# Performance work log

Measured on AMD Instinct MI355X. Metric: run time of the kernel, lower is better.

Reference implementation:

```python
import jax, jax.numpy as jnp
import numpy as np

B, L, C = 2048, 2048, 16
F = L // 2                 # num_freqs = 1024
H = 4 * F                  # multi_factor * num_freqs = 4096
P = int(len(np.unique(L // np.arange(1, F + 1))))  # n patch sizes = 88
SCALE = 0.02
NOISE_EPS = 0.01


def setup_inputs() -> dict:
    key = jax.random.key(0)
    ks = jax.random.split(key, 10)
    return {
        "x": jax.random.normal(ks[0], (B, L, C), jnp.float32),
        "w_start": SCALE * jax.random.normal(ks[1], (C, 1), jnp.float32),
        "b_start": SCALE * jax.random.normal(ks[2], (1,), jnp.float32),
        "w1": SCALE * jax.random.normal(ks[3], (2, F, H), jnp.float32),
        "b1": SCALE * jax.random.normal(ks[4], (2, H), jnp.float32),
        "w2": SCALE * jax.random.normal(ks[5], (2, H, F), jnp.float32),
        "b2": SCALE * jax.random.normal(ks[6], (2, F), jnp.float32),
        "w_gate": SCALE * jax.random.normal(ks[7], (F, P), jnp.float32),
        "w_noise": SCALE * jax.random.normal(ks[8], (F, P), jnp.float32),
        "noise_z": jax.random.normal(ks[9], (B, P), jnp.float32),
        "top_k": 3,
    }


def reference(x, w_start, b_start, w1, b1, w2, b2, w_gate, w_noise, noise_z, top_k):
    # start_fc: [B, L, C] -> [B, L, 1] -> [B, 1, L]
    v = (jnp.einsum("blc,co->blo", x, w_start) + b_start).transpose(0, 2, 1)
    # rfft (ortho), drop DC bin -> [B, 1, F] complex
    xf = jnp.fft.rfft(v, axis=-1, norm="ortho")[:, :, 1:]
    xr, xi = jnp.real(xf), jnp.imag(xf)
    # complex 2-layer MLP in frequency domain
    o1r = jax.nn.relu(jnp.einsum("bdi,io->bdo", xr, w1[0]) - jnp.einsum("bdi,io->bdo", xi, w1[1]) + b1[0])
    o1i = jax.nn.relu(jnp.einsum("bdi,io->bdo", xi, w1[0]) + jnp.einsum("bdi,io->bdo", xr, w1[1]) + b1[1])
    o2r = jnp.einsum("bdo,of->bdf", o1r, w2[0]) - jnp.einsum("bdo,of->bdf", o1i, w2[1]) + b2[0]
    o2i = jnp.einsum("bdo,of->bdf", o1i, w2[0]) + jnp.einsum("bdo,of->bdf", o1r, w2[1]) + b2[1]
    amp = jnp.sqrt(o2r * o2r + o2i * o2i)[:, 0, :]  # [B, F]
    # router logits with (training) noise injection
    clean_logits = amp @ w_gate                      # [B, P]
    noise_std = jax.nn.softplus(amp @ w_noise) + NOISE_EPS
    logits = clean_logits + noise_z * noise_std
    # top-k -> softmax over top-k -> scatter into sparse gates
    top_w, top_i = jax.lax.top_k(logits, top_k)
    top_w = jax.nn.softmax(top_w, axis=-1)
    rows = jnp.arange(logits.shape[0])[:, None]
    gates = jnp.zeros_like(logits).at[rows, top_i].set(top_w)
    return gates
```

## Files before the change

### kernel.cpp

```cpp
#include <hip/hip_runtime.h>
#include <hip/hip_bf16.h>
#include <math.h>

#define B_DIM 2048
#define L_DIM 2048
#define F_DIM 1024
#define H_DIM 4096
#define P_DIM 88

typedef unsigned short u16;
typedef short bf16x8 __attribute__((ext_vector_type(8)));
typedef float f32x4 __attribute__((ext_vector_type(4)));

__device__ __forceinline__ u16 f2bf(float x) {
    unsigned u = __float_as_uint(x);
    return (u16)((u + 0x7fffu + ((u >> 16) & 1u)) >> 16);
}
__device__ __forceinline__ float bf2f(u16 h) {
    return __uint_as_float(((unsigned)h) << 16);
}

__device__ __forceinline__ void gload_lds16(const void* g, void* l) {
    unsigned loff = (unsigned)(uintptr_t)l;
    __builtin_amdgcn_global_load_lds(
        reinterpret_cast<const __attribute__((address_space(1))) void*>(
            reinterpret_cast<uintptr_t>(g)),
        reinterpret_cast<__attribute__((address_space(3))) void*>(loff),
        16, 0, 0);
}

__global__ __launch_bounds__(256) void fft_kernel(
    const float* __restrict__ x, const float* __restrict__ w_start,
    const float* __restrict__ b_start, u16* __restrict__ A1)
{
    __shared__ float re[2048];
    __shared__ float im[2048];
    __shared__ float twr[1024];
    __shared__ float twi[1024];
    int b = blockIdx.x;
    const size_t row0 = (size_t)(2 * b) * 2048;

    const float4* wp = (const float4*)w_start;
    float4 w0 = wp[0], w1 = wp[1], w2 = wp[2], w3 = wp[3];
    float bs = b_start[0];

    for (int i = threadIdx.x; i < 1024; i += 256) {
        float ang = -6.283185307179586f * ((float)i / 2048.0f);
        sincosf(ang, &twi[i], &twr[i]);
    }

    for (int l = threadIdx.x; l < 2048; l += 256) {
        const float4* xp0 = (const float4*)(x + (row0 + l) * 16);
        const float4* xp1 = (const float4*)(x + (row0 + 2048 + l) * 16);
        float4 a0 = xp0[0], a1 = xp0[1], a2 = xp0[2], a3 = xp0[3];
        float4 c0 = xp1[0], c1 = xp1[1], c2 = xp1[2], c3 = xp1[3];
        float va = bs, vb = bs;
        va += a0.x * w0.x + a0.y * w0.y + a0.z * w0.z + a0.w * w0.w;
        va += a1.x * w1.x + a1.y * w1.y + a1.z * w1.z + a1.w * w1.w;
        va += a2.x * w2.x + a2.y * w2.y + a2.z * w2.z + a2.w * w2.w;
        va += a3.x * w3.x + a3.y * w3.y + a3.z * w3.z + a3.w * w3.w;
        vb += c0.x * w0.x + c0.y * w0.y + c0.z * w0.z + c0.w * w0.w;
        vb += c1.x * w1.x + c1.y * w1.y + c1.z * w1.z + c1.w * w1.w;
        vb += c2.x * w2.x + c2.y * w2.y + c2.z * w2.z + c2.w * w2.w;
        vb += c3.x * w3.x + c3.y * w3.y + c3.z * w3.z + c3.w * w3.w;
        unsigned j = __brev((unsigned)l) >> 21;
        re[j] = va;
        im[j] = vb;
    }
    __syncthreads();

    for (int s = 1; s <= 11; s++) {
        int half = 1 << (s - 1);
        for (int t = threadIdx.x; t < 1024; t += 256) {
            int j = t & (half - 1);
            int base = (t >> (s - 1)) << s;
            int idx = j << (11 - s);
            float wr = twr[idx], wi = twi[idx];
            int i0 = base + j, i1 = i0 + half;
            float br = re[i1], bi = im[i1];
            float tr = br * wr - bi * wi;
            float ti = br * wi + bi * wr;
            float ar = re[i0], ai = im[i0];
            re[i0] = ar + tr; im[i0] = ai + ti;
            re[i1] = ar - tr; im[i1] = ai - ti;
        }
        __syncthreads();
    }

    const float sc = 0.5f * 0.022097086912079612f;
    u16* r0 = A1 + (size_t)(2 * b) * 4096;
    u16* r1 = r0 + 4096;
    for (int t = threadIdx.x; t < 1024; t += 256) {
        int k = t + 1;
        int nk = 2048 - k;
        float Zr = re[k], Zi = im[k], Yr = re[nk], Yi = im[nk];
        float Ar = (Zr + Yr) * sc;
        float Ai = (Zi - Yi) * sc;
        float Br = (Zi + Yi) * sc;
        float Bi = (Yr - Zr) * sc;
        u16 h, lo;
        h = f2bf(Ar); lo = f2bf(Ar - bf2f(h)); r0[t] = h; r0[1024 + t] = lo;
        h = f2bf(Ai); lo = f2bf(Ai - bf2f(h)); r0[2048 + t] = h; r0[3072 + t] = lo;
        h = f2bf(Br); lo = f2bf(Br - bf2f(h)); r1[t] = h; r1[1024 + t] = lo;
        h = f2bf(Bi); lo = f2bf(Bi - bf2f(h)); r1[2048 + t] = h; r1[3072 + t] = lo;
    }
}

__global__ __launch_bounds__(256) void conv_bt_kernel(
    const float* __restrict__ w, u16* __restrict__ BT, int Kc, int Nh)
{
    __shared__ float t0[32][33];
    __shared__ float t1[32][33];
    int k0 = blockIdx.x * 32, n0 = blockIdx.y * 32;
    int tx = threadIdx.x, ty = threadIdx.y;
    const float* w0 = w;
    const float* w1 = w + (size_t)Kc * Nh;

#pragma unroll
    for (int i = 0; i < 4; i++) {
        int k = k0 + ty + 8 * i;
        t0[ty + 8 * i][tx] = w0[(size_t)k * Nh + n0 + tx];
        t1[ty + 8 * i][tx] = w1[(size_t)k * Nh + n0 + tx];
    }
    __syncthreads();

    size_t K4 = 4 * (size_t)Kc;
    int k = k0 + tx;
#pragma unroll
    for (int i = 0; i < 4; i++) {
        int nl = ty + 8 * i;
        int n = n0 + nl;
        float br = t0[tx][nl];
        float bi = t1[tx][nl];
        u16 brh = f2bf(br); u16 brl = f2bf(br - bf2f(brh));
        float nbi = -bi;
        u16 nih = f2bf(nbi); u16 nil = f2bf(nbi - bf2f(nih));
        u16 pih = f2bf(bi);  u16 pil = f2bf(bi - bf2f(pih));
        u16* rowr = BT + (size_t)n * K4;
        rowr[0 * Kc + k] = brh; rowr[1 * Kc + k] = brl;
        rowr[2 * Kc + k] = nih; rowr[3 * Kc + k] = nil;
        u16* rowi = BT + (size_t)(Nh + n) * K4;
        rowi[0 * Kc + k] = pih; rowi[1 * Kc + k] = pil;
        rowi[2 * Kc + k] = brh; rowi[3 * Kc + k] = brl;
    }
}

extern __shared__ char smem8p[];

#define MFMA16(ACC0, ACC1, ACC2, ACC3, A0, A1, A2, A3, B0, B1, B2, B3)           \
    ACC0[0] = __builtin_amdgcn_mfma_f32_16x16x32_bf16(A0, B0, ACC0[0], 0, 0, 0); \
    ACC0[1] = __builtin_amdgcn_mfma_f32_16x16x32_bf16(A0, B1, ACC0[1], 0, 0, 0); \
    ACC0[2] = __builtin_amdgcn_mfma_f32_16x16x32_bf16(A0, B2, ACC0[2], 0, 0, 0); \
    ACC0[3] = __builtin_amdgcn_mfma_f32_16x16x32_bf16(A0, B3, ACC0[3], 0, 0, 0); \
    ACC1[0] = __builtin_amdgcn_mfma_f32_16x16x32_bf16(A1, B0, ACC1[0], 0, 0, 0); \
    ACC1[1] = __builtin_amdgcn_mfma_f32_16x16x32_bf16(A1, B1, ACC1[1], 0, 0, 0); \
    ACC1[2] = __builtin_amdgcn_mfma_f32_16x16x32_bf16(A1, B2, ACC1[2], 0, 0, 0); \
    ACC1[3] = __builtin_amdgcn_mfma_f32_16x16x32_bf16(A1, B3, ACC1[3], 0, 0, 0); \
    ACC2[0] = __builtin_amdgcn_mfma_f32_16x16x32_bf16(A2, B0, ACC2[0], 0, 0, 0); \
    ACC2[1] = __builtin_amdgcn_mfma_f32_16x16x32_bf16(A2, B1, ACC2[1], 0, 0, 0); \
    ACC2[2] = __builtin_amdgcn_mfma_f32_16x16x32_bf16(A2, B2, ACC2[2], 0, 0, 0); \
    ACC2[3] = __builtin_amdgcn_mfma_f32_16x16x32_bf16(A2, B3, ACC2[3], 0, 0, 0); \
    ACC3[0] = __builtin_amdgcn_mfma_f32_16x16x32_bf16(A3, B0, ACC3[0], 0, 0, 0); \
    ACC3[1] = __builtin_amdgcn_mfma_f32_16x16x32_bf16(A3, B1, ACC3[1], 0, 0, 0); \
    ACC3[2] = __builtin_amdgcn_mfma_f32_16x16x32_bf16(A3, B2, ACC3[2], 0, 0, 0); \
    ACC3[3] = __builtin_amdgcn_mfma_f32_16x16x32_bf16(A3, B3, ACC3[3], 0, 0, 0);

template <int EPI, int SWZ>
__global__ __launch_bounds__(512, 2) void gemm8p(
    const u16* __restrict__ A, const u16* __restrict__ B,
    const float* __restrict__ biasL, const float* __restrict__ biasR,
    u16* __restrict__ OutU, float* __restrict__ P01, float* __restrict__ P23,
    int Kc, int KcLog, int NH, int nt)
{
    char* ldsA = smem8p;
    char* ldsB = smem8p + 65536;

    const int tid = threadIdx.x;
    const int w = tid >> 6, lane = tid & 63;
    const int wr = w >> 2, wc = w & 3;
    const int fr = lane & 15, kb = lane >> 4;

    int bx, by, z;
    if (SWZ == 1) {
        int b = blockIdx.x;
        int xcd = b & 7, idx = b >> 3;
        bx = 4 * xcd + (idx & 3);
        by = idx >> 2;
        z = 0;
    } else if (SWZ == 2) {
        int b = blockIdx.x;
        by = b & 7;
        int s = b >> 3;
        bx = s & 7;
        z = s >> 3;
    } else {
        bx = blockIdx.x; by = blockIdx.y; z = blockIdx.z;
    }
    const int n0 = bx * 256, m0 = by * 256;
    const size_t K4 = 4 * (size_t)Kc;

    const int srow = tid >> 2;
    const int lk8 = (((tid & 3) ^ ((tid >> 3) & 3))) * 8;
    const int wb = (tid >> 6) * 1024;

    const int laneOff = fr * 64 + ((kb ^ ((fr >> 1) & 3)) << 4);

    f32x4 acc[8][4];
#pragma unroll
    for (int i = 0; i < 8; i++)
#pragma unroll
        for (int j = 0; j < 4; j++)
            acc[i][j] = (f32x4){0.f, 0.f, 0.f, 0.f};

    const int t0 = z * nt, te = t0 + nt;

    auto colA = [&](int t) {
        int k0 = t << 5;
        int seg = k0 >> KcLog, kk = k0 & (Kc - 1);
        int r3 = seg >= 3 ? seg - 3 : seg;
        int bs = seg >= 3 ? 2 : 0;
        return (bs + (r3 == 1 ? 1 : 0)) * Kc + kk;
    };
    auto colB = [&](int t) {
        int k0 = t << 5;
        int seg = k0 >> KcLog, kk = k0 & (Kc - 1);
        int r3 = seg >= 3 ? seg - 3 : seg;
        int bs = seg >= 3 ? 2 : 0;
        return (bs + (r3 == 2 ? 1 : 0)) * Kc + kk;
    };
    auto stageA = [&](int t) {
        const u16* src = A + (size_t)(m0 + srow) * K4 + colA(t) + lk8;
        char* dst = ldsA + (t & 3) * 16384 + wb;
        gload_lds16(src, dst);
        gload_lds16(src + (size_t)128 * K4, dst + 8192);
    };
    auto stageB = [&](int t) {
        const u16* src = B + (size_t)(n0 + srow) * K4 + colB(t) + lk8;
        char* dst = ldsB + (t & 3) * 16384 + wb;
        gload_lds16(src, dst);
        gload_lds16(src + (size_t)128 * K4, dst + 8192);
    };
    auto aBase = [&](int t) -> const char* {
        return ldsA + (t & 3) * 16384 + wr * 8192 + laneOff;
    };
    auto bBase = [&](int t) -> const char* {
        return ldsB + (t & 3) * 16384 + wc * 4096 + laneOff;
    };

    stageA(t0); stageB(t0);
    if (t0 + 1 < te) { stageA(t0 + 1); stageB(t0 + 1); }
    if (t0 + 1 < te) asm volatile("s_waitcnt vmcnt(4)" ::: "memory");
    else             asm volatile("s_waitcnt vmcnt(0)" ::: "memory");
    asm volatile("s_barrier" ::: "memory");

    bf16x8 b0, b1, b2, b3, a0, a1, a2, a3;
    {
        const char* aS = aBase(t0);
        const char* bS = bBase(t0);
        b0 = *(const bf16x8*)(bS + 0 * 1024);
        b1 = *(const bf16x8*)(bS + 1 * 1024);
        b2 = *(const bf16x8*)(bS + 2 * 1024);
        b3 = *(const bf16x8*)(bS + 3 * 1024);
        a0 = *(const bf16x8*)(aS + 0 * 1024);
        a1 = *(const bf16x8*)(aS + 1 * 1024);
        a2 = *(const bf16x8*)(aS + 2 * 1024);
        a3 = *(const bf16x8*)(aS + 3 * 1024);
    }

    for (int t = t0; t < te; ++t) {
        const bool haveStage = (t + 2 < te);
        const bool haveNext  = (t + 1 < te);

        if (haveStage) { stageA(t + 2); stageB(t + 2); }

        const char* aS = aBase(t);
        bf16x8 c0 = *(const bf16x8*)(aS + 4096 + 0 * 1024);
        bf16x8 c1 = *(const bf16x8*)(aS + 4096 + 1 * 1024);
        bf16x8 c2 = *(const bf16x8*)(aS + 4096 + 2 * 1024);
        bf16x8 c3 = *(const bf16x8*)(aS + 4096 + 3 * 1024);

        __builtin_amdgcn_s_setprio(1);
        MFMA16(acc[0], acc[1], acc[2], acc[3], a0, a1, a2, a3, b0, b1, b2, b3)
        __builtin_amdgcn_s_setprio(0);

        if (haveStage) asm volatile("s_waitcnt vmcnt(4)" ::: "memory");
        else           asm volatile("s_waitcnt vmcnt(0)" ::: "memory");
        asm volatile("s_barrier" ::: "memory");

        if (haveNext) {
            const char* aN = aBase(t + 1);
            a0 = *(const bf16x8*)(aN + 0 * 1024);
            a1 = *(const bf16x8*)(aN + 1 * 1024);
            a2 = *(const bf16x8*)(aN + 2 * 1024);
            a3 = *(const bf16x8*)(aN + 3 * 1024);
        }

        __builtin_amdgcn_s_setprio(1);
        MFMA16(acc[4], acc[5], acc[6], acc[7], c0, c1, c2, c3, b0, b1, b2, b3)
        __builtin_amdgcn_s_setprio(0);

        if (haveNext) {
            const char* bN = bBase(t + 1);
            b0 = *(const bf16x8*)(bN + 0 * 1024);
            b1 = *(const bf16x8*)(bN + 1 * 1024);
            b2 = *(const bf16x8*)(bN + 2 * 1024);
            b3 = *(const bf16x8*)(bN + 3 * 1024);
        }
    }

    const int fq = kb;
#pragma unroll
    for (int nj = 0; nj < 4; nj++) {
        int n = n0 + wc * 64 + nj * 16 + fr;
        if (EPI == 0) {
            bool left = (n < NH);
            int nn = left ? n : (n - NH);
            float bias = left ? biasL[n] : biasR[nn];
#pragma unroll
            for (int mi = 0; mi < 8; mi++) {
                int mb = m0 + wr * 128 + mi * 16 + fq * 4;
#pragma unroll
                for (int r = 0; r < 4; r++) {
                    float val = fmaxf(acc[mi][nj][r] + bias, 0.f);
                    u16 h = f2bf(val);
                    u16 lo = f2bf(val - bf2f(h));
                    size_t rb = (size_t)(mb + r) * (4 * (size_t)NH);
                    if (left) { OutU[rb + nn] = h; OutU[rb + NH + nn] = lo; }
                    else { OutU[rb + 2 * (size_t)NH + nn] = h; OutU[rb + 3 * (size_t)NH + nn] = lo; }
                }
            }
        } else {
            const size_t PSZ = (size_t)2048 * 2048;
            float* Out = (z < 2) ? (P01 + (size_t)z * PSZ) : (P23 + (size_t)(z - 2) * PSZ);
#pragma unroll
            for (int mi = 0; mi < 8; mi++) {
                int mb = m0 + wr * 128 + mi * 16 + fq * 4;
#pragma unroll
                for (int r = 0; r < 4; r++)
                    Out[(size_t)(mb + r) * 2048 + n] = acc[mi][nj][r];
            }
        }
    }
}

__global__ __launch_bounds__(256) void router_kernel(
    const float* __restrict__ P01, const float* __restrict__ P23, int ZK,
    const float* __restrict__ b2,
    const float* __restrict__ w_gate, const float* __restrict__ w_noise,
    const float* __restrict__ noise_z, float* __restrict__ gates)
{
    __shared__ float s_amp[8][1024];
    __shared__ float s_dot[8][176];
    __shared__ float s_lg[8][88];
    __shared__ int   s_idx[8][3];
    __shared__ float s_val[8][3];

    const int tid = threadIdx.x;
    const int r0 = blockIdx.x * 8;
    const size_t PSZ = (size_t)2048 * 2048;

    for (int idx = tid; idx < 8 * 1024; idx += 256) {
        int row = idx >> 10, i = idx & 1023;
        size_t roff = (size_t)(r0 + row) * 2048;
        float orr = b2[i];
        float oii = b2[1024 + i];
        for (int zz = 0; zz < ZK; zz++) {
            const float* Pz = ((zz < 2) ? (P01 + (size_t)zz * PSZ)
                                        : (P23 + (size_t)(zz - 2) * PSZ)) + roff;
            orr += Pz[i];
            oii += Pz[1024 + i];
        }
        s_amp[row][i] = sqrtf(orr * orr + oii * oii);
    }
    __syncthreads();

    for (int idx = tid; idx < 8 * 176; idx += 256) {
        int row = idx / 176, c = idx % 176;
        const float* wcol = (c < 88) ? (w_gate + c) : (w_noise + (c - 88));
        float s = 0.f;
        const float4* av = (const float4*)s_amp[row];
        for (int k4 = 0; k4 < 256; k4++) {
            float4 a = av[k4];
            int k = k4 * 4;
            s = fmaf(a.x, wcol[(size_t)(k + 0) * 88], s);
            s = fmaf(a.y, wcol[(size_t)(k + 1) * 88], s);
            s = fmaf(a.z, wcol[(size_t)(k + 2) * 88], s);
            s = fmaf(a.w, wcol[(size_t)(k + 3) * 88], s);
        }
        s_dot[row][c] = s;
    }
    __syncthreads();

    for (int idx = tid; idx < 8 * 88; idx += 256) {
        int row = idx / 88, c = idx % 88;
        float cn = s_dot[row][88 + c];
        float ns = (cn > 20.f) ? cn : log1pf(expf(cn));
        ns += 0.01f;
        s_lg[row][c] = s_dot[row][c] + noise_z[(size_t)(r0 + row) * 88 + c] * ns;
    }
    __syncthreads();

    if (tid < 8) {
        int i0 = -1, i1 = -1, i2 = -1;
        float v0 = -1e30f, v1 = -1e30f, v2 = -1e30f;
        for (int i = 0; i < P_DIM; i++) {
            float t = s_lg[tid][i];
            if (t > v0) { v0 = t; i0 = i; }
        }
        for (int i = 0; i < P_DIM; i++) {
            if (i == i0) continue;
            float t = s_lg[tid][i];
            if (t > v1) { v1 = t; i1 = i; }
        }
        for (int i = 0; i < P_DIM; i++) {
            if (i == i0 || i == i1) continue;
            float t = s_lg[tid][i];
            if (t > v2) { v2 = t; i2 = i; }
        }
        s_idx[tid][0] = i0; s_idx[tid][1] = i1; s_idx[tid][2] = i2;
        s_val[tid][0] = v0; s_val[tid][1] = v1; s_val[tid][2] = v2;
    }
    __syncthreads();

    for (int idx = tid; idx < 8 * 88; idx += 256) {
        int row = idx / 88, c = idx % 88;
        float m = s_val[row][0];
        float e0 = expf(s_val[row][0] - m);
        float e1 = expf(s_val[row][1] - m);
        float e2 = expf(s_val[row][2] - m);
        float inv = 1.f / (e0 + e1 + e2);
        float g = 0.f;
        if (c == s_idx[row][0]) g = e0 * inv;
        else if (c == s_idx[row][1]) g = e1 * inv;
        else if (c == s_idx[row][2]) g = e2 * inv;
        gates[(size_t)(r0 + row) * 88 + c] = g;
    }
}

extern "C" void kernel_launch(void* const* d_in, const int* in_sizes, int n_in,
                              void* d_out, int out_size, void* d_ws, size_t ws_size,
                              hipStream_t stream)
{
    const float* x       = (const float*)d_in[0];
    const float* w_start = (const float*)d_in[1];
    const float* b_start = (const float*)d_in[2];
    const float* w1      = (const float*)d_in[3];
    const float* b1      = (const float*)d_in[4];
    const float* w2      = (const float*)d_in[5];
    const float* b2      = (const float*)d_in[6];
    const float* w_gate  = (const float*)d_in[7];
    const float* w_noise = (const float*)d_in[8];
    const float* noise_z = (const float*)d_in[9];
    float* gates = (float*)d_out;

    const size_t MB = 1024 * 1024;
    char* base = (char*)d_ws;
    u16*  A1   = (u16*)(base + 16 * MB);
    u16*  BT   = (u16*)(base + 32 * MB);
    u16*  A2   = (u16*)(base + 96 * MB);
    float* P01 = (float*)base;
    float* P23 = (float*)(base + 160 * MB);

    int ZK = (ws_size >= (size_t)192 * MB) ? 4 : 2;

    hipFuncSetAttribute(reinterpret_cast<const void*>(&gemm8p<0, 1>),
                        hipFuncAttributeMaxDynamicSharedMemorySize, 131072);
    hipFuncSetAttribute(reinterpret_cast<const void*>(&gemm8p<1, 2>),
                        hipFuncAttributeMaxDynamicSharedMemorySize, 131072);

    fft_kernel<<<B_DIM / 2, 256, 0, stream>>>(x, w_start, b_start, A1);

    conv_bt_kernel<<<dim3(F_DIM / 32, H_DIM / 32), dim3(32, 8), 0, stream>>>(
        w1, BT, F_DIM, H_DIM);
    gemm8p<0, 1><<<256, 512, 131072, stream>>>(
        A1, BT, b1, b1 + H_DIM, A2, nullptr, nullptr, F_DIM, 10, H_DIM, 192);

    conv_bt_kernel<<<dim3(H_DIM / 32, F_DIM / 32), dim3(32, 8), 0, stream>>>(
        w2, BT, H_DIM, F_DIM);
    gemm8p<1, 2><<<64 * ZK, 512, 131072, stream>>>(
        A2, BT, nullptr, nullptr, nullptr, P01, P23, H_DIM, 12, F_DIM, 768 / ZK);

    router_kernel<<<B_DIM / 8, 256, 0, stream>>>(
        P01, P23, ZK, b2, w_gate, w_noise, noise_z, gates);
}
```

Baseline: 600.5 us.

## Load GEMM B operand directly from global in MFMA-ready layout, bypassing LDS

The weight-conversion kernel now writes the split-bf16 B matrix in a k-chunked layout of 8-element vectors per column, so each lane can fetch its MFMA B fragment with a single 16-byte global load. The GEMM drops the B LDS staging buffer and its async copies, prefetches B one tile ahead in registers, and unrolls the K loop by two to ping-pong the register sets. This halves dynamic shared memory and removes B LDS traffic, but each wave now issues its own uncoalesced-ish global loads for B with no cross-wave reuse, and assumes an even tile count per block.

```diff
diff --git a/kernel.cpp b/kernel.cpp
--- a/kernel.cpp
+++ b/kernel.cpp
@@ -107,7 +107,7 @@
 }
 
 __global__ __launch_bounds__(256) void conv_bt_kernel(
-    const float* __restrict__ w, u16* __restrict__ BT, int Kc, int Nh)
+    const float* __restrict__ w, u16* __restrict__ BTk, int Kc, int Nh)
 {
     __shared__ float t0[32][33];
     __shared__ float t1[32][33];
@@ -124,8 +124,9 @@
     }
     __syncthreads();
 
-    size_t K4 = 4 * (size_t)Kc;
+    const size_t N2 = 2 * (size_t)Nh;
     int k = k0 + tx;
+    int ke = k & 7;
 #pragma unroll
     for (int i = 0; i < 4; i++) {
         int nl = ty + 8 * i;
@@ -136,18 +137,27 @@
         float nbi = -bi;
         u16 nih = f2bf(nbi); u16 nil = f2bf(nbi - bf2f(nih));
         u16 pih = f2bf(bi);  u16 pil = f2bf(bi - bf2f(pih));
-        u16* rowr = BT + (size_t)n * K4;
-        rowr[0 * Kc + k] = brh; rowr[1 * Kc + k] = brl;
-        rowr[2 * Kc + k] = nih; rowr[3 * Kc + k] = nil;
-        u16* rowi = BT + (size_t)(Nh + n) * K4;
-        rowi[0 * Kc + k] = pih; rowi[1 * Kc + k] = pil;
-        rowi[2 * Kc + k] = brh; rowi[3 * Kc + k] = brl;
+        size_t c8b = (size_t)(k >> 3);
+        size_t cstep = (size_t)(Kc >> 3);
+        size_t ur = 0, ui = 0;
+        ur = (c8b + 0 * cstep) * N2 + n;
+        BTk[ur * 8 + ke] = brh;
+        BTk[(c8b + 1 * cstep) * N2 * 8 + (size_t)n * 8 + ke] = brl;
+        BTk[(c8b + 2 * cstep) * N2 * 8 + (size_t)n * 8 + ke] = nih;
+        BTk[(c8b + 3 * cstep) * N2 * 8 + (size_t)n * 8 + ke] = nil;
+        BTk[ur * 8 + ke] = brh;
+        size_t nr = (size_t)(Nh + n);
+        BTk[(c8b + 0 * cstep) * N2 * 8 + nr * 8 + ke] = pih;
+        BTk[(c8b + 1 * cstep) * N2 * 8 + nr * 8 + ke] = pil;
+        BTk[(c8b + 2 * cstep) * N2 * 8 + nr * 8 + ke] = brh;
+        BTk[(c8b + 3 * cstep) * N2 * 8 + nr * 8 + ke] = brl;
+        (void)ui;
     }
 }
 
 extern __shared__ char smem8p[];
 
-#define MFMA16(ACC0, ACC1, ACC2, ACC3, A0, A1, A2, A3, B0, B1, B2, B3)           \
+#define MFMA16X(ACC0, ACC1, ACC2, ACC3, A0, A1, A2, A3, B0, B1, B2, B3)          \
     ACC0[0] = __builtin_amdgcn_mfma_f32_16x16x32_bf16(A0, B0, ACC0[0], 0, 0, 0); \
     ACC0[1] = __builtin_amdgcn_mfma_f32_16x16x32_bf16(A0, B1, ACC0[1], 0, 0, 0); \
     ACC0[2] = __builtin_amdgcn_mfma_f32_16x16x32_bf16(A0, B2, ACC0[2], 0, 0, 0); \
@@ -165,6 +175,41 @@
     ACC3[2] = __builtin_amdgcn_mfma_f32_16x16x32_bf16(A3, B2, ACC3[2], 0, 0, 0); \
     ACC3[3] = __builtin_amdgcn_mfma_f32_16x16x32_bf16(A3, B3, ACC3[3], 0, 0, 0);
 
+#define GTILE(T, BC0, BC1, BC2, BC3, BN0, BN1, BN2, BN3)                          \
+    {                                                                             \
+        const bool haveStage = ((T) + 2 < te);                                    \
+        const bool haveNext  = ((T) + 1 < te);                                    \
+        if (haveNext) {                                                           \
+            size_t u = (size_t)(unsigned)(colB((T) + 1) >> 3) * N2 + laneB;       \
+            BN0 = BK[u];      BN1 = BK[u + 16];                                   \
+            BN2 = BK[u + 32]; BN3 = BK[u + 48];                                   \
+        }                                                                         \
+        if (haveStage) stageA((T) + 2);                                           \
+        const char* aS = aBase(T);                                                \
+        bf16x8 c0 = *(const bf16x8*)(aS + 4096 + 0 * 1024);                       \
+        bf16x8 c1 = *(const bf16x8*)(aS + 4096 + 1 * 1024);                       \
+        bf16x8 c2 = *(const bf16x8*)(aS + 4096 + 2 * 1024);                       \
+        bf16x8 c3 = *(const bf16x8*)(aS + 4096 + 3 * 1024);                       \
+        __builtin_amdgcn_s_setprio(1);                                            \
+        MFMA16X(acc[0], acc[1], acc[2], acc[3], a0, a1, a2, a3,                   \
+                BC0, BC1, BC2, BC3)                                               \
+        __builtin_amdgcn_s_setprio(0);                                            \
+        if (haveStage) asm volatile("s_waitcnt vmcnt(2)" ::: "memory");           \
+        else           asm volatile("s_waitcnt vmcnt(0)" ::: "memory");           \
+        asm volatile("s_barrier" ::: "memory");                                   \
+        if (haveNext) {                                                           \
+            const char* aN = aBase((T) + 1);                                      \
+            a0 = *(const bf16x8*)(aN + 0 * 1024);                                 \
+            a1 = *(const bf16x8*)(aN + 1 * 1024);                                 \
+            a2 = *(const bf16x8*)(aN + 2 * 1024);                                 \
+            a3 = *(const bf16x8*)(aN + 3 * 1024);                                 \
+        }                                                                         \
+        __builtin_amdgcn_s_setprio(1);                                            \
+        MFMA16X(acc[4], acc[5], acc[6], acc[7], c0, c1, c2, c3,                   \
+                BC0, BC1, BC2, BC3)                                               \
+        __builtin_amdgcn_s_setprio(0);                                            \
+    }
+
 template <int EPI, int SWZ>
 __global__ __launch_bounds__(512, 2) void gemm8p(
     const u16* __restrict__ A, const u16* __restrict__ B,
@@ -173,7 +218,6 @@
     int Kc, int KcLog, int NH, int nt)
 {
     char* ldsA = smem8p;
-    char* ldsB = smem8p + 65536;
 
     const int tid = threadIdx.x;
     const int w = tid >> 6, lane = tid & 63;
@@ -198,12 +242,16 @@
     }
     const int n0 = bx * 256, m0 = by * 256;
     const size_t K4 = 4 * (size_t)Kc;
+    const size_t N2 = 2 * (size_t)NH;
 
     const int srow = tid >> 2;
     const int lk8 = (((tid & 3) ^ ((tid >> 3) & 3))) * 8;
     const int wb = (tid >> 6) * 1024;
 
     const int laneOff = fr * 64 + ((kb ^ ((fr >> 1) & 3)) << 4);
+
+    const bf16x8* BK = (const bf16x8*)B;
+    const size_t laneB = (size_t)kb * N2 + (size_t)(n0 + wc * 64 + fr);
 
     f32x4 acc[8][4];
 #pragma unroll
@@ -234,78 +282,33 @@
         gload_lds16(src, dst);
         gload_lds16(src + (size_t)128 * K4, dst + 8192);
     };
-    auto stageB = [&](int t) {
-        const u16* src = B + (size_t)(n0 + srow) * K4 + colB(t) + lk8;
-        char* dst = ldsB + (t & 3) * 16384 + wb;
-        gload_lds16(src, dst);
-        gload_lds16(src + (size_t)128 * K4, dst + 8192);
-    };
     auto aBase = [&](int t) -> const char* {
         return ldsA + (t & 3) * 16384 + wr * 8192 + laneOff;
     };
-    auto bBase = [&](int t) -> const char* {
-        return ldsB + (t & 3) * 16384 + wc * 4096 + laneOff;
-    };
-
-    stageA(t0); stageB(t0);
-    if (t0 + 1 < te) { stageA(t0 + 1); stageB(t0 + 1); }
-    if (t0 + 1 < te) asm volatile("s_waitcnt vmcnt(4)" ::: "memory");
-    else             asm volatile("s_waitcnt vmcnt(0)" ::: "memory");
+
+    bf16x8 bc0, bc1, bc2, bc3, bn0, bn1, bn2, bn3;
+    {
+        size_t u = (size_t)(unsigned)(colB(t0) >> 3) * N2 + laneB;
+        bc0 = BK[u];      bc1 = BK[u + 16];
+        bc2 = BK[u + 32]; bc3 = BK[u + 48];
+    }
+    stageA(t0);
+    stageA(t0 + 1);
+    asm volatile("s_waitcnt vmcnt(2)" ::: "memory");
     asm volatile("s_barrier" ::: "memory");
 
-    bf16x8 b0, b1, b2, b3, a0, a1, a2, a3;
+    bf16x8 a0, a1, a2, a3;
     {
         const char* aS = aBase(t0);
-        const char* bS = bBase(t0);
-        b0 = *(const bf16x8*)(bS + 0 * 1024);
-        b1 = *(const bf16x8*)(bS + 1 * 1024);
-        b2 = *(const bf16x8*)(bS + 2 * 1024);
-        b3 = *(const bf16x8*)(bS + 3 * 1024);
         a0 = *(const bf16x8*)(aS + 0 * 1024);
         a1 = *(const bf16x8*)(aS + 1 * 1024);
         a2 = *(const bf16x8*)(aS + 2 * 1024);
         a3 = *(const bf16x8*)(aS + 3 * 1024);
     }
 
-    for (int t = t0; t < te; ++t) {
-        const bool haveStage = (t + 2 < te);
-        const bool haveNext  = (t + 1 < te);
-
-        if (haveStage) { stageA(t + 2); stageB(t + 2); }
-
-        const char* aS = aBase(t);
-        bf16x8 c0 = *(const bf16x8*)(aS + 4096 + 0 * 1024);
-        bf16x8 c1 = *(const bf16x8*)(aS + 4096 + 1 * 1024);
-        bf16x8 c2 = *(const bf16x8*)(aS + 4096 + 2 * 1024);
-        bf16x8 c3 = *(const bf16x8*)(aS + 4096 + 3 * 1024);
-
-        __builtin_amdgcn_s_setprio(1);
-        MFMA16(acc[0], acc[1], acc[2], acc[3], a0, a1, a2, a3, b0, b1, b2, b3)
-        __builtin_amdgcn_s_setprio(0);
-
-        if (haveStage) asm volatile("s_waitcnt vmcnt(4)" ::: "memory");
-        else           asm volatile("s_waitcnt vmcnt(0)" ::: "memory");
-        asm volatile("s_barrier" ::: "memory");
-
-        if (haveNext) {
-            const char* aN = aBase(t + 1);
-            a0 = *(const bf16x8*)(aN + 0 * 1024);
-            a1 = *(const bf16x8*)(aN + 1 * 1024);
-            a2 = *(const bf16x8*)(aN + 2 * 1024);
-            a3 = *(const bf16x8*)(aN + 3 * 1024);
-        }
-
-        __builtin_amdgcn_s_setprio(1);
-        MFMA16(acc[4], acc[5], acc[6], acc[7], c0, c1, c2, c3, b0, b1, b2, b3)
-        __builtin_amdgcn_s_setprio(0);
-
-        if (haveNext) {
-            const char* bN = bBase(t + 1);
-            b0 = *(const bf16x8*)(bN + 0 * 1024);
-            b1 = *(const bf16x8*)(bN + 1 * 1024);
-            b2 = *(const bf16x8*)(bN + 2 * 1024);
-            b3 = *(const bf16x8*)(bN + 3 * 1024);
-        }
+    for (int t = t0; t < te; t += 2) {
+        GTILE(t,     bc0, bc1, bc2, bc3, bn0, bn1, bn2, bn3)
+        GTILE(t + 1, bn0, bn1, bn2, bn3, bc0, bc1, bc2, bc3)
     }
 
     const int fq = kb;
@@ -464,20 +467,20 @@
     int ZK = (ws_size >= (size_t)192 * MB) ? 4 : 2;
 
     hipFuncSetAttribute(reinterpret_cast<const void*>(&gemm8p<0, 1>),
-                        hipFuncAttributeMaxDynamicSharedMemorySize, 131072);
+                        hipFuncAttributeMaxDynamicSharedMemorySize, 65536);
     hipFuncSetAttribute(reinterpret_cast<const void*>(&gemm8p<1, 2>),
-                        hipFuncAttributeMaxDynamicSharedMemorySize, 131072);
+                        hipFuncAttributeMaxDynamicSharedMemorySize, 65536);
 
     fft_kernel<<<B_DIM / 2, 256, 0, stream>>>(x, w_start, b_start, A1);
 
     conv_bt_kernel<<<dim3(F_DIM / 32, H_DIM / 32), dim3(32, 8), 0, stream>>>(
         w1, BT, F_DIM, H_DIM);
-    gemm8p<0, 1><<<256, 512, 131072, stream>>>(
+    gemm8p<0, 1><<<256, 512, 65536, stream>>>(
         A1, BT, b1, b1 + H_DIM, A2, nullptr, nullptr, F_DIM, 10, H_DIM, 192);
 
     conv_bt_kernel<<<dim3(H_DIM / 32, F_DIM / 32), dim3(32, 8), 0, stream>>>(
         w2, BT, H_DIM, F_DIM);
-    gemm8p<1, 2><<<64 * ZK, 512, 131072, stream>>>(
+    gemm8p<1, 2><<<64 * ZK, 512, 65536, stream>>>(
         A2, BT, nullptr, nullptr, nullptr, P01, P23, H_DIM, 12, F_DIM, 768 / ZK);
 
     router_kernel<<<B_DIM / 8, 256, 0, stream>>>(
```

New measurement: 650.7 us. 1.08x slower.
